# Performance work log

Measured on AMD Instinct MI355X. Metric: run time of the kernel, lower is better.

## Reference

```python
import jax, jax.numpy as jnp
import numpy as np

B, C, W, H = 4, 512, 64, 64
CK = C // 8  # channels // k


def setup_inputs() -> dict:
    key = jax.random.key(0)
    ks = jax.random.split(key, 10)
    s = 0.02
    return {
        "x": jax.random.normal(ks[0], (B, C, W, H), jnp.float32),
        "wf": jax.random.normal(ks[1], (CK, C), jnp.float32) * s,
        "bf": jax.random.normal(ks[2], (CK,), jnp.float32) * s,
        "wg": jax.random.normal(ks[3], (CK, C), jnp.float32) * s,
        "bg": jax.random.normal(ks[4], (CK,), jnp.float32) * s,
        "wh": jax.random.normal(ks[5], (CK, C), jnp.float32) * s,
        "bh": jax.random.normal(ks[6], (CK,), jnp.float32) * s,
        "wv": jax.random.normal(ks[7], (C, CK), jnp.float32) * s,
        "bv": jax.random.normal(ks[8], (C,), jnp.float32) * s,
        "gamma": jax.random.normal(ks[9], (1,), jnp.float32) * 0.1,
    }


def reference(x, wf, bf, wg, bg, wh, bh, wv, bv, gamma):
    b, c, w, h = x.shape
    n = w * h  # location_num
    xf = x.reshape(b, c, n)  # (B, C, N)
    # conv1x1 projections == per-location matmuls
    f = jnp.einsum('oc,bcn->bon', wf, xf) + bf[None, :, None]  # (B, CK, N)
    g = jnp.einsum('oc,bcn->bon', wg, xf) + bg[None, :, None]
    hh = jnp.einsum('oc,bcn->bon', wh, xf) + bh[None, :, None]
    # beta[b, i, j] = sum_c f[b,c,i] * g[b,c,j]; softmax over dim=1 (i axis)
    beta = jax.nn.softmax(jnp.einsum('bcn,bcm->bnm', f, g), axis=1)  # (B, N, N)
    h2 = jnp.einsum('bcn,bnm->bcm', hh, beta)  # (B, CK, N)
    o = jnp.einsum('oc,bcn->bon', wv, h2) + bv[None, :, None]  # (B, C, N)
    y = gamma[0] * o + xf
    return y.reshape(b, c, w, h)
```

## Files before the change

### kernel.cpp

```cpp
#include <hip/hip_runtime.h>
#include <stdint.h>

#define B_ 4
#define C_ 512
#define N_ 4096
#define D_ 64
#define LOG2E 1.4426950408889634f

typedef __attribute__((ext_vector_type(8))) short short8;
typedef __attribute__((ext_vector_type(4))) float f32x4;
typedef __attribute__((ext_vector_type(16))) float f32x16;
typedef unsigned short ushort_t;

static __device__ __forceinline__ ushort_t f2bf(float f) {
    union { float f; uint32_t u; } v; v.f = f;
    uint32_t u = v.u;
    uint32_t r = u + 0x7FFFu + ((u >> 16) & 1u);
    return (ushort_t)(r >> 16);
}
static __device__ __forceinline__ float bf2f(uint32_t u) {
    union { uint32_t u; float f; } v; v.u = u << 16;
    return v.f;
}
static __device__ __forceinline__ uint32_t cvtpk_bf16(float lo, float hi) {
    uint32_t r;
    asm("v_cvt_pk_bf16_f32 %0, %1, %2" : "=v"(r) : "v"(lo), "v"(hi));
    return r;
}
static __device__ __forceinline__ void gl16(const ushort_t* g, ushort_t* l) {
    __builtin_amdgcn_global_load_lds(
        (const __attribute__((address_space(1))) void*)g,
        (__attribute__((address_space(3))) void*)l, 16, 0, 0);
}

__global__ __launch_bounds__(512) void proj_fgh(
    const float* __restrict__ x,
    const float* __restrict__ wf, const float* __restrict__ bf,
    const float* __restrict__ wg, const float* __restrict__ bg,
    const float* __restrict__ wh, const float* __restrict__ bh,
    ushort_t* __restrict__ Ftf, ushort_t* __restrict__ Gt,
    ushort_t* __restrict__ Vtf)
{
    const int b    = blockIdx.y;
    const int tile = blockIdx.x;
    const int n0   = tile * 64;
    const int tid  = threadIdx.x;
    const int wv   = tid >> 6;
    const int mw   = wv & 3;
    const int hi   = wv >> 2;
    const int lane = tid & 63;
    const int g    = lane >> 4;
    const int r    = lane & 15;

    __shared__ ushort_t As[64][40];
    __shared__ ushort_t Bs[192][40];

    f32x4 acc[6];
    #pragma unroll
    for (int t = 0; t < 6; ++t) acc[t] = (f32x4){0.f, 0.f, 0.f, 0.f};

    const int ka = tid >> 4;
    const int mb = (tid & 15) * 4;
    const int kb = (tid & 7) * 4;
    const int ow = tid >> 3;

    const float* xp  = x  + ((size_t)b * C_ + ka) * N_ + n0 + mb;
    const float* wp0 = wf + (size_t)ow * C_ + kb;
    const float* wp1 = wg + (size_t)ow * C_ + kb;
    const float* wp2 = wh + (size_t)ow * C_ + kb;

    float4 xa = *(const float4*)xp;
    float4 w0 = *(const float4*)wp0;
    float4 w1 = *(const float4*)wp1;
    float4 w2 = *(const float4*)wp2;

    for (int k0 = 0; k0 < C_; k0 += 32) {
        As[mb + 0][ka] = f2bf(xa.x);
        As[mb + 1][ka] = f2bf(xa.y);
        As[mb + 2][ka] = f2bf(xa.z);
        As[mb + 3][ka] = f2bf(xa.w);
        {
            uint2 p0, p1, p2;
            p0.x = cvtpk_bf16(w0.x, w0.y); p0.y = cvtpk_bf16(w0.z, w0.w);
            p1.x = cvtpk_bf16(w1.x, w1.y); p1.y = cvtpk_bf16(w1.z, w1.w);
            p2.x = cvtpk_bf16(w2.x, w2.y); p2.y = cvtpk_bf16(w2.z, w2.w);
            *(uint2*)&Bs[ow][kb]       = p0;
            *(uint2*)&Bs[64 + ow][kb]  = p1;
            *(uint2*)&Bs[128 + ow][kb] = p2;
        }
        if (k0 + 32 < C_) {
            xa = *(const float4*)(xp + (size_t)(k0 + 32) * N_);
            w0 = *(const float4*)(wp0 + k0 + 32);
            w1 = *(const float4*)(wp1 + k0 + 32);
            w2 = *(const float4*)(wp2 + k0 + 32);
        }
        __syncthreads();
        short8 a = *(const short8*)&As[16 * mw + r][8 * g];
        __builtin_amdgcn_s_setprio(1);
        #pragma unroll
        for (int tt = 0; tt < 6; ++tt) {
            const int T = hi * 6 + tt;
            short8 bbv = *(const short8*)&Bs[T * 16 + r][8 * g];
            acc[tt] = __builtin_amdgcn_mfma_f32_16x16x32_bf16(a, bbv, acc[tt], 0, 0, 0);
        }
        __builtin_amdgcn_s_setprio(0);
        __syncthreads();
    }

    #pragma unroll
    for (int u = 0; u < 2; ++u) {
        const int tt = hi ? u : (4 + u);
        const int og = hi ? (32 + u * 16 + r) : (u * 16 + r);
        const float bvv = bg[og];
        #pragma unroll
        for (int j = 0; j < 4; ++j) {
            const int loc = n0 + 16 * mw + 4 * g + j;
            Gt[((size_t)b * N_ + loc) * D_ + og] = f2bf(acc[tt][j] + bvv);
        }
    }

    ushort_t (*bb)[72] = (ushort_t(*)[72])Bs;

    if (hi == 0) {
        #pragma unroll
        for (int tt = 0; tt < 4; ++tt) {
            const int o = tt * 16 + r;
            const float bvv = bf[o];
            #pragma unroll
            for (int j = 0; j < 4; ++j)
                bb[16 * mw + 4 * g + j][o] = f2bf((acc[tt][j] + bvv) * LOG2E);
        }
    }
    __syncthreads();
    {
        const int f  = wv;
        const int cc = f >> 2, s = f & 3;
        short8 v = *(const short8*)&bb[32 * cc + (lane & 31)][16 * s + 8 * (lane >> 5)];
        *(short8*)&Ftf[(((size_t)b * 64 + tile) * 8 + f) * 512 + lane * 8] = v;
    }
    __syncthreads();

    if (hi == 1) {
        #pragma unroll
        for (int tt = 2; tt < 6; ++tt) {
            const int o = (tt - 2) * 16 + r;
            const float bvv = bh[o];
            #pragma unroll
            for (int j = 0; j < 4; ++j)
                bb[16 * mw + 4 * g + j][o] = f2bf(acc[tt][j] + bvv);
        }
    }
    __syncthreads();
    {
        const int f   = wv;
        const int cc  = f >> 2, sub = (f >> 1) & 1, dt = f & 1;
        const int h2l = lane >> 5;
        short8 v;
        #pragma unroll
        for (int e = 0; e < 8; ++e) {
            const int i = 32 * cc + 16 * sub + (e & 3) + 8 * (e >> 2) + 4 * h2l;
            v[e] = (short)bb[i][32 * dt + (lane & 31)];
        }
        *(short8*)&Vtf[(((size_t)b * 64 + tile) * 8 + f) * 512 + lane * 8] = v;
    }
}

__global__ __launch_bounds__(256, 4) void attn(
    const ushort_t* __restrict__ Ftf, const ushort_t* __restrict__ Gt,
    const ushort_t* __restrict__ Vtf, ushort_t* __restrict__ Ot,
    ushort_t* __restrict__ Op, float* __restrict__ ml, int ksplit)
{
    const int b    = blockIdx.z;
    const int part = blockIdx.y;
    const int tid  = threadIdx.x;
    const int wave = tid >> 6;
    const int lane = tid & 63;
    const int l31  = lane & 31;
    const int h2   = lane >> 5;
    const int j0   = blockIdx.x * 128 + wave * 32;
    const int NT   = (N_ / ksplit) / 64;
    const int kt0  = part * NT;

    __shared__ __align__(16) ushort_t Ks[2][4096];
    __shared__ __align__(16) ushort_t Vs[2][4096];

    const ushort_t* qrow = Gt + ((size_t)b * N_ + j0 + l31) * D_ + 8 * h2;
    const short8 qf0 = *(const short8*)(qrow);
    const short8 qf1 = *(const short8*)(qrow + 16);
    const short8 qf2 = *(const short8*)(qrow + 32);
    const short8 qf3 = *(const short8*)(qrow + 48);

    const ushort_t* Kt = Ftf + ((size_t)b * 64 + kt0) * 4096;
    const ushort_t* Vt = Vtf + ((size_t)b * 64 + kt0) * 4096;

    f32x16 oA, oB;
    #pragma unroll
    for (int q = 0; q < 16; ++q) { oA[q] = 0.f; oB[q] = 0.f; }
    float l_run = 0.f;

    gl16(Kt + tid * 8,         &Ks[0][tid * 8]);
    gl16(Kt + (tid + 256) * 8, &Ks[0][(tid + 256) * 8]);
    gl16(Vt + tid * 8,         &Vs[0][tid * 8]);
    gl16(Vt + (tid + 256) * 8, &Vs[0][(tid + 256) * 8]);

    int buf = 0;
    for (int t = 0; t < NT; ++t) {
        __syncthreads();
        if (t + 1 < NT) {
            const ushort_t* kg = Kt + (size_t)(t + 1) * 4096;
            const ushort_t* vg = Vt + (size_t)(t + 1) * 4096;
            const int nb = buf ^ 1;
            gl16(kg + tid * 8,         &Ks[nb][tid * 8]);
            gl16(kg + (tid + 256) * 8, &Ks[nb][(tid + 256) * 8]);
            gl16(vg + tid * 8,         &Vs[nb][tid * 8]);
            gl16(vg + (tid + 256) * 8, &Vs[nb][(tid + 256) * 8]);
        }
        #pragma unroll
        for (int cc = 0; cc < 2; ++cc) {
            const ushort_t* kb0 = &Ks[buf][cc * 2048];
            f32x16 sx;
            #pragma unroll
            for (int q = 0; q < 16; ++q) sx[q] = 0.f;
            __builtin_amdgcn_s_setprio(1);
            {
                const short8 k0 = *(const short8*)(kb0 + 0 * 512 + lane * 8);
                sx = __builtin_amdgcn_mfma_f32_32x32x16_bf16(k0, qf0, sx, 0, 0, 0);
                const short8 k1 = *(const short8*)(kb0 + 1 * 512 + lane * 8);
                sx = __builtin_amdgcn_mfma_f32_32x32x16_bf16(k1, qf1, sx, 0, 0, 0);
                const short8 k2 = *(const short8*)(kb0 + 2 * 512 + lane * 8);
                sx = __builtin_amdgcn_mfma_f32_32x32x16_bf16(k2, qf2, sx, 0, 0, 0);
                const short8 k3 = *(const short8*)(kb0 + 3 * 512 + lane * 8);
                sx = __builtin_amdgcn_mfma_f32_32x32x16_bf16(k3, qf3, sx, 0, 0, 0);
            }
            __builtin_amdgcn_s_setprio(0);

            uint32_t pw[8];
            float cs = 0.f;
            #pragma unroll
            for (int q = 0; q < 8; ++q) {
                const float pa = __builtin_amdgcn_exp2f(sx[2 * q]);
                const float pb = __builtin_amdgcn_exp2f(sx[2 * q + 1]);
                cs += pa + pb;
                pw[q] = cvtpk_bf16(pa, pb);
            }
            l_run += cs;

            union { uint32_t w[4]; short8 v; } p0u, p1u;
            p0u.w[0] = pw[0]; p0u.w[1] = pw[1]; p0u.w[2] = pw[2]; p0u.w[3] = pw[3];
            p1u.w[0] = pw[4]; p1u.w[1] = pw[5]; p1u.w[2] = pw[6]; p1u.w[3] = pw[7];

            const ushort_t* vb0 = &Vs[buf][cc * 2048];
            __builtin_amdgcn_s_setprio(1);
            {
                const short8 v00 = *(const short8*)(vb0 + 0 * 512 + lane * 8);
                oA = __builtin_amdgcn_mfma_f32_32x32x16_bf16(v00, p0u.v, oA, 0, 0, 0);
                const short8 v01 = *(const short8*)(vb0 + 1 * 512 + lane * 8);
                oB = __builtin_amdgcn_mfma_f32_32x32x16_bf16(v01, p0u.v, oB, 0, 0, 0);
                const short8 v10 = *(const short8*)(vb0 + 2 * 512 + lane * 8);
                oA = __builtin_amdgcn_mfma_f32_32x32x16_bf16(v10, p1u.v, oA, 0, 0, 0);
                const short8 v11 = *(const short8*)(vb0 + 3 * 512 + lane * 8);
                oB = __builtin_amdgcn_mfma_f32_32x32x16_bf16(v11, p1u.v, oB, 0, 0, 0);
            }
            __builtin_amdgcn_s_setprio(0);
        }
        buf ^= 1;
    }

    const float lt = l_run + __shfl_xor(l_run, 32);

    if (ksplit == 1) {
        const float inv = 1.0f / lt;
        ushort_t* orow = Ot + ((size_t)b * N_ + j0 + l31) * D_;
        #pragma unroll
        for (int q = 0; q < 4; ++q) {
            const int d0 = 8 * q + 4 * h2;
            uint2 ua, ub;
            ua.x = cvtpk_bf16(oA[4 * q] * inv,     oA[4 * q + 1] * inv);
            ua.y = cvtpk_bf16(oA[4 * q + 2] * inv, oA[4 * q + 3] * inv);
            *(uint2*)&orow[d0] = ua;
            ub.x = cvtpk_bf16(oB[4 * q] * inv,     oB[4 * q + 1] * inv);
            ub.y = cvtpk_bf16(oB[4 * q + 2] * inv, oB[4 * q + 3] * inv);
            *(uint2*)&orow[32 + d0] = ub;
        }
    } else {
        ushort_t* orow = Op + (((size_t)b * ksplit + part) * N_ + j0 + l31) * D_;
        #pragma unroll
        for (int q = 0; q < 4; ++q) {
            const int d0 = 8 * q + 4 * h2;
            uint2 ua, ub;
            ua.x = cvtpk_bf16(oA[4 * q],     oA[4 * q + 1]);
            ua.y = cvtpk_bf16(oA[4 * q + 2], oA[4 * q + 3]);
            *(uint2*)&orow[d0] = ua;
            ub.x = cvtpk_bf16(oB[4 * q],     oB[4 * q + 1]);
            ub.y = cvtpk_bf16(oB[4 * q + 2], oB[4 * q + 3]);
            *(uint2*)&orow[32 + d0] = ub;
        }
        if (h2 == 0)
            ml[((size_t)b * ksplit + part) * N_ + j0 + l31] = lt;
    }
}

__global__ __launch_bounds__(256) void reduce_attn(
    const ushort_t* __restrict__ Op, const float* __restrict__ ml,
    ushort_t* __restrict__ Ot, int ksplit)
{
    const int tid = blockIdx.x * 256 + threadIdx.x;
    const int d4 = (tid & 15) * 4;
    const int j  = (tid >> 4) & (N_ - 1);
    const int b  = tid >> 16;

    float L = 0.f, v0 = 0.f, v1 = 0.f, v2 = 0.f, v3 = 0.f;
    for (int p = 0; p < ksplit; ++p) {
        const size_t base = ((size_t)b * ksplit + p) * N_ + j;
        L += ml[base];
        uint2 u = *(const uint2*)&Op[base * D_ + d4];
        v0 += bf2f(u.x & 0xffffu);
        v1 += bf2f(u.x >> 16);
        v2 += bf2f(u.y & 0xffffu);
        v3 += bf2f(u.y >> 16);
    }
    const float inv = 1.0f / L;
    uint2 o;
    o.x = cvtpk_bf16(v0 * inv, v1 * inv);
    o.y = cvtpk_bf16(v2 * inv, v3 * inv);
    *(uint2*)&Ot[((size_t)b * N_ + j) * D_ + d4] = o;
}

__global__ __launch_bounds__(256) void outproj(
    const ushort_t* __restrict__ Ot, const float* __restrict__ wv,
    const float* __restrict__ bv, const float* __restrict__ gamma,
    const float* __restrict__ x, float* __restrict__ y)
{
    const int b    = blockIdx.z;
    const int wave = threadIdx.x >> 6;
    const int lane = threadIdx.x & 63;
    const int g    = lane >> 4;
    const int r    = lane & 15;
    const int co0  = blockIdx.y * 64 + wave * 16;
    const int n0   = blockIdx.x * 64;

    const float* wrow = wv + (size_t)(co0 + r) * D_ + 8 * g;
    short8 a0, a1;
    #pragma unroll
    for (int j = 0; j < 8; ++j) {
        a0[j] = (short)f2bf(wrow[j]);
        a1[j] = (short)f2bf(wrow[32 + j]);
    }

    f32x4 acc[4];
    #pragma unroll
    for (int t = 0; t < 4; ++t) acc[t] = (f32x4){0.f, 0.f, 0.f, 0.f};

    #pragma unroll
    for (int t = 0; t < 4; ++t) {
        const ushort_t* op = Ot + ((size_t)b * N_ + n0 + 16 * t + r) * D_ + 8 * g;
        short8 b0 = *(const short8*)op;
        short8 b1 = *(const short8*)(op + 32);
        acc[t] = __builtin_amdgcn_mfma_f32_16x16x32_bf16(a0, b0, acc[t], 0, 0, 0);
        acc[t] = __builtin_amdgcn_mfma_f32_16x16x32_bf16(a1, b1, acc[t], 0, 0, 0);
    }

    const float gm = *gamma;
    #pragma unroll
    for (int t = 0; t < 4; ++t) {
        #pragma unroll
        for (int j = 0; j < 4; ++j) {
            const int co = co0 + 4 * g + j;
            const int n  = n0 + 16 * t + r;
            const size_t idx = ((size_t)b * C_ + co) * N_ + n;
            y[idx] = gm * (acc[t][j] + bv[co]) + x[idx];
        }
    }
}

extern "C" void kernel_launch(void* const* d_in, const int* in_sizes, int n_in,
                              void* d_out, int out_size, void* d_ws, size_t ws_size,
                              hipStream_t stream) {
    const float* x     = (const float*)d_in[0];
    const float* wf    = (const float*)d_in[1];
    const float* bf    = (const float*)d_in[2];
    const float* wg    = (const float*)d_in[3];
    const float* bg    = (const float*)d_in[4];
    const float* wh    = (const float*)d_in[5];
    const float* bh    = (const float*)d_in[6];
    const float* wv    = (const float*)d_in[7];
    const float* bv    = (const float*)d_in[8];
    const float* gamma = (const float*)d_in[9];
    float* y = (float*)d_out;

    const size_t plane = (size_t)B_ * N_ * D_;
    ushort_t* Ftf = (ushort_t*)d_ws;
    ushort_t* Gt  = Ftf + plane;
    ushort_t* Vtf = Gt + plane;
    ushort_t* Ot  = Vtf + plane;
    ushort_t* Op  = Ot + plane;

    int KS = 8;
    while (KS > 1) {
        const size_t need = 4 * plane * 2 + (size_t)KS * plane * 2
                          + (size_t)B_ * KS * N_ * sizeof(float);
        if (need <= ws_size) break;
        KS >>= 1;
    }
    float* ml = (float*)(Op + (size_t)KS * plane);

    proj_fgh<<<dim3(N_ / 64, B_), 512, 0, stream>>>(
        x, wf, bf, wg, bg, wh, bh, Ftf, Gt, Vtf);
    attn<<<dim3(N_ / 128, KS, B_), 256, 0, stream>>>(
        Ftf, Gt, Vtf, Ot, Op, ml, KS);
    if (KS > 1)
        reduce_attn<<<(B_ * N_ * 16) / 256, 256, 0, stream>>>(Op, ml, Ot, KS);
    outproj<<<dim3(N_ / 64, C_ / 64, B_), 256, 0, stream>>>(Ot, wv, bv, gamma, x, y);
}
```

Baseline: 65.47 us.

## Process two query tiles per wave in attention to reuse K/V LDS loads

Each wave now handles 64 query columns (two 32-wide tiles) instead of 32, so every K and V fragment read from shared memory feeds two MFMAs. The block covers 256 queries and the grid halves, cutting LDS and global K/V traffic per unit of work. Register pressure roughly doubles for accumulators, so launch bounds drop occupancy to 2 blocks per SIMD-group, and fewer blocks may underfill the GPU. The split-K reduce kernel is also widened to 8 bf16 elements per thread with 128-bit loads.

```diff
diff --git a/kernel.cpp b/kernel.cpp
--- a/kernel.cpp
+++ b/kernel.cpp
@@ -165,7 +165,7 @@
     }
 }
 
-__global__ __launch_bounds__(256, 4) void attn(
+__global__ __launch_bounds__(256, 2) void attn(
     const ushort_t* __restrict__ Ftf, const ushort_t* __restrict__ Gt,
     const ushort_t* __restrict__ Vtf, ushort_t* __restrict__ Ot,
     ushort_t* __restrict__ Op, float* __restrict__ ml, int ksplit)
@@ -177,26 +177,31 @@
     const int lane = tid & 63;
     const int l31  = lane & 31;
     const int h2   = lane >> 5;
-    const int j0   = blockIdx.x * 128 + wave * 32;
+    const int j0   = blockIdx.x * 256 + wave * 64;
     const int NT   = (N_ / ksplit) / 64;
     const int kt0  = part * NT;
 
     __shared__ __align__(16) ushort_t Ks[2][4096];
     __shared__ __align__(16) ushort_t Vs[2][4096];
 
-    const ushort_t* qrow = Gt + ((size_t)b * N_ + j0 + l31) * D_ + 8 * h2;
-    const short8 qf0 = *(const short8*)(qrow);
-    const short8 qf1 = *(const short8*)(qrow + 16);
-    const short8 qf2 = *(const short8*)(qrow + 32);
-    const short8 qf3 = *(const short8*)(qrow + 48);
+    const ushort_t* qrowA = Gt + ((size_t)b * N_ + j0 + l31) * D_ + 8 * h2;
+    const ushort_t* qrowB = qrowA + (size_t)32 * D_;
+    const short8 qA0 = *(const short8*)(qrowA);
+    const short8 qA1 = *(const short8*)(qrowA + 16);
+    const short8 qA2 = *(const short8*)(qrowA + 32);
+    const short8 qA3 = *(const short8*)(qrowA + 48);
+    const short8 qB0 = *(const short8*)(qrowB);
+    const short8 qB1 = *(const short8*)(qrowB + 16);
+    const short8 qB2 = *(const short8*)(qrowB + 32);
+    const short8 qB3 = *(const short8*)(qrowB + 48);
 
     const ushort_t* Kt = Ftf + ((size_t)b * 64 + kt0) * 4096;
     const ushort_t* Vt = Vtf + ((size_t)b * 64 + kt0) * 4096;
 
-    f32x16 oA, oB;
-    #pragma unroll
-    for (int q = 0; q < 16; ++q) { oA[q] = 0.f; oB[q] = 0.f; }
-    float l_run = 0.f;
+    f32x16 oAA, oBA, oAB, oBB;
+    #pragma unroll
+    for (int q = 0; q < 16; ++q) { oAA[q] = 0.f; oBA[q] = 0.f; oAB[q] = 0.f; oBB[q] = 0.f; }
+    float lA = 0.f, lB = 0.f;
 
     gl16(Kt + tid * 8,         &Ks[0][tid * 8]);
     gl16(Kt + (tid + 256) * 8, &Ks[0][(tid + 256) * 8]);
@@ -218,85 +223,119 @@
         #pragma unroll
         for (int cc = 0; cc < 2; ++cc) {
             const ushort_t* kb0 = &Ks[buf][cc * 2048];
-            f32x16 sx;
+            f32x16 sxA, sxB;
             #pragma unroll
-            for (int q = 0; q < 16; ++q) sx[q] = 0.f;
+            for (int q = 0; q < 16; ++q) { sxA[q] = 0.f; sxB[q] = 0.f; }
             __builtin_amdgcn_s_setprio(1);
             {
                 const short8 k0 = *(const short8*)(kb0 + 0 * 512 + lane * 8);
-                sx = __builtin_amdgcn_mfma_f32_32x32x16_bf16(k0, qf0, sx, 0, 0, 0);
+                sxA = __builtin_amdgcn_mfma_f32_32x32x16_bf16(k0, qA0, sxA, 0, 0, 0);
+                sxB = __builtin_amdgcn_mfma_f32_32x32x16_bf16(k0, qB0, sxB, 0, 0, 0);
                 const short8 k1 = *(const short8*)(kb0 + 1 * 512 + lane * 8);
-                sx = __builtin_amdgcn_mfma_f32_32x32x16_bf16(k1, qf1, sx, 0, 0, 0);
+                sxA = __builtin_amdgcn_mfma_f32_32x32x16_bf16(k1, qA1, sxA, 0, 0, 0);
+                sxB = __builtin_amdgcn_mfma_f32_32x32x16_bf16(k1, qB1, sxB, 0, 0, 0);
                 const short8 k2 = *(const short8*)(kb0 + 2 * 512 + lane * 8);
-                sx = __builtin_amdgcn_mfma_f32_32x32x16_bf16(k2, qf2, sx, 0, 0, 0);
+                sxA = __builtin_amdgcn_mfma_f32_32x32x16_bf16(k2, qA2, sxA, 0, 0, 0);
+                sxB = __builtin_amdgcn_mfma_f32_32x32x16_bf16(k2, qB2, sxB, 0, 0, 0);
                 const short8 k3 = *(const short8*)(kb0 + 3 * 512 + lane * 8);
-                sx = __builtin_amdgcn_mfma_f32_32x32x16_bf16(k3, qf3, sx, 0, 0, 0);
+                sxA = __builtin_amdgcn_mfma_f32_32x32x16_bf16(k3, qA3, sxA, 0, 0, 0);
+                sxB = __builtin_amdgcn_mfma_f32_32x32x16_bf16(k3, qB3, sxB, 0, 0, 0);
             }
             __builtin_amdgcn_s_setprio(0);
 
-            uint32_t pw[8];
-            float cs = 0.f;
+            uint32_t pwA[8], pwB[8];
+            float cA0 = 0.f, cA1 = 0.f, cB0 = 0.f, cB1 = 0.f;
             #pragma unroll
             for (int q = 0; q < 8; ++q) {
-                const float pa = __builtin_amdgcn_exp2f(sx[2 * q]);
-                const float pb = __builtin_amdgcn_exp2f(sx[2 * q + 1]);
-                cs += pa + pb;
-                pw[q] = cvtpk_bf16(pa, pb);
+                const float a0 = __builtin_amdgcn_exp2f(sxA[2 * q]);
+                const float a1 = __builtin_amdgcn_exp2f(sxA[2 * q + 1]);
+                cA0 += a0; cA1 += a1;
+                pwA[q] = cvtpk_bf16(a0, a1);
+                const float b0 = __builtin_amdgcn_exp2f(sxB[2 * q]);
+                const float b1 = __builtin_amdgcn_exp2f(sxB[2 * q + 1]);
+                cB0 += b0; cB1 += b1;
+                pwB[q] = cvtpk_bf16(b0, b1);
             }
-            l_run += cs;
-
-            union { uint32_t w[4]; short8 v; } p0u, p1u;
-            p0u.w[0] = pw[0]; p0u.w[1] = pw[1]; p0u.w[2] = pw[2]; p0u.w[3] = pw[3];
-            p1u.w[0] = pw[4]; p1u.w[1] = pw[5]; p1u.w[2] = pw[6]; p1u.w[3] = pw[7];
+            lA += cA0 + cA1;
+            lB += cB0 + cB1;
+
+            union { uint32_t w[4]; short8 v; } pA0u, pA1u, pB0u, pB1u;
+            pA0u.w[0] = pwA[0]; pA0u.w[1] = pwA[1]; pA0u.w[2] = pwA[2]; pA0u.w[3] = pwA[3];
+            pA1u.w[0] = pwA[4]; pA1u.w[1] = pwA[5]; pA1u.w[2] = pwA[6]; pA1u.w[3] = pwA[7];
+            pB0u.w[0] = pwB[0]; pB0u.w[1] = pwB[1]; pB0u.w[2] = pwB[2]; pB0u.w[3] = pwB[3];
+            pB1u.w[0] = pwB[4]; pB1u.w[1] = pwB[5]; pB1u.w[2] = pwB[6]; pB1u.w[3] = pwB[7];
 
             const ushort_t* vb0 = &Vs[buf][cc * 2048];
             __builtin_amdgcn_s_setprio(1);
             {
                 const short8 v00 = *(const short8*)(vb0 + 0 * 512 + lane * 8);
-                oA = __builtin_amdgcn_mfma_f32_32x32x16_bf16(v00, p0u.v, oA, 0, 0, 0);
+                oAA = __builtin_amdgcn_mfma_f32_32x32x16_bf16(v00, pA0u.v, oAA, 0, 0, 0);
+                oAB = __builtin_amdgcn_mfma_f32_32x32x16_bf16(v00, pB0u.v, oAB, 0, 0, 0);
                 const short8 v01 = *(const short8*)(vb0 + 1 * 512 + lane * 8);
-                oB = __builtin_amdgcn_mfma_f32_32x32x16_bf16(v01, p0u.v, oB, 0, 0, 0);
+                oBA = __builtin_amdgcn_mfma_f32_32x32x16_bf16(v01, pA0u.v, oBA, 0, 0, 0);
+                oBB = __builtin_amdgcn_mfma_f32_32x32x16_bf16(v01, pB0u.v, oBB, 0, 0, 0);
                 const short8 v10 = *(const short8*)(vb0 + 2 * 512 + lane * 8);
-                oA = __builtin_amdgcn_mfma_f32_32x32x16_bf16(v10, p1u.v, oA, 0, 0, 0);
+                oAA = __builtin_amdgcn_mfma_f32_32x32x16_bf16(v10, pA1u.v, oAA, 0, 0, 0);
+                oAB = __builtin_amdgcn_mfma_f32_32x32x16_bf16(v10, pB1u.v, oAB, 0, 0, 0);
                 const short8 v11 = *(const short8*)(vb0 + 3 * 512 + lane * 8);
-                oB = __builtin_amdgcn_mfma_f32_32x32x16_bf16(v11, p1u.v, oB, 0, 0, 0);
+                oBA = __builtin_amdgcn_mfma_f32_32x32x16_bf16(v11, pA1u.v, oBA, 0, 0, 0);
+                oBB = __builtin_amdgcn_mfma_f32_32x32x16_bf16(v11, pB1u.v, oBB, 0, 0, 0);
             }
             __builtin_amdgcn_s_setprio(0);
         }
         buf ^= 1;
     }
 
-    const float lt = l_run + __shfl_xor(l_run, 32);
+    const float ltA = lA + __shfl_xor(lA, 32);
+    const float ltB = lB + __shfl_xor(lB, 32);
 
     if (ksplit == 1) {
-        const float inv = 1.0f / lt;
-        ushort_t* orow = Ot + ((size_t)b * N_ + j0 + l31) * D_;
+        const float invA = 1.0f / ltA;
+        const float invB = 1.0f / ltB;
+        ushort_t* orowA = Ot + ((size_t)b * N_ + j0 + l31) * D_;
+        ushort_t* orowB = orowA + (size_t)32 * D_;
         #pragma unroll
         for (int q = 0; q < 4; ++q) {
             const int d0 = 8 * q + 4 * h2;
-            uint2 ua, ub;
-            ua.x = cvtpk_bf16(oA[4 * q] * inv,     oA[4 * q + 1] * inv);
-            ua.y = cvtpk_bf16(oA[4 * q + 2] * inv, oA[4 * q + 3] * inv);
-            *(uint2*)&orow[d0] = ua;
-            ub.x = cvtpk_bf16(oB[4 * q] * inv,     oB[4 * q + 1] * inv);
-            ub.y = cvtpk_bf16(oB[4 * q + 2] * inv, oB[4 * q + 3] * inv);
-            *(uint2*)&orow[32 + d0] = ub;
+            uint2 u;
+            u.x = cvtpk_bf16(oAA[4 * q] * invA,     oAA[4 * q + 1] * invA);
+            u.y = cvtpk_bf16(oAA[4 * q + 2] * invA, oAA[4 * q + 3] * invA);
+            *(uint2*)&orowA[d0] = u;
+            u.x = cvtpk_bf16(oBA[4 * q] * invA,     oBA[4 * q + 1] * invA);
+            u.y = cvtpk_bf16(oBA[4 * q + 2] * invA, oBA[4 * q + 3] * invA);
+            *(uint2*)&orowA[32 + d0] = u;
+            u.x = cvtpk_bf16(oAB[4 * q] * invB,     oAB[4 * q + 1] * invB);
+            u.y = cvtpk_bf16(oAB[4 * q + 2] * invB, oAB[4 * q + 3] * invB);
+            *(uint2*)&orowB[d0] = u;
+            u.x = cvtpk_bf16(oBB[4 * q] * invB,     oBB[4 * q + 1] * invB);
+            u.y = cvtpk_bf16(oBB[4 * q + 2] * invB, oBB[4 * q + 3] * invB);
+            *(uint2*)&orowB[32 + d0] = u;
         }
     } else {
-        ushort_t* orow = Op + (((size_t)b * ksplit + part) * N_ + j0 + l31) * D_;
+        ushort_t* orowA = Op + (((size_t)b * ksplit + part) * N_ + j0 + l31) * D_;
+        ushort_t* orowB = orowA + (size_t)32 * D_;
         #pragma unroll
         for (int q = 0; q < 4; ++q) {
             const int d0 = 8 * q + 4 * h2;
-            uint2 ua, ub;
-            ua.x = cvtpk_bf16(oA[4 * q],     oA[4 * q + 1]);
-            ua.y = cvtpk_bf16(oA[4 * q + 2], oA[4 * q + 3]);
-            *(uint2*)&orow[d0] = ua;
-            ub.x = cvtpk_bf16(oB[4 * q],     oB[4 * q + 1]);
-            ub.y = cvtpk_bf16(oB[4 * q + 2], oB[4 * q + 3]);
-            *(uint2*)&orow[32 + d0] = ub;
-        }
-        if (h2 == 0)
-            ml[((size_t)b * ksplit + part) * N_ + j0 + l31] = lt;
+            uint2 u;
+            u.x = cvtpk_bf16(oAA[4 * q],     oAA[4 * q + 1]);
+            u.y = cvtpk_bf16(oAA[4 * q + 2], oAA[4 * q + 3]);
+            *(uint2*)&orowA[d0] = u;
+            u.x = cvtpk_bf16(oBA[4 * q],     oBA[4 * q + 1]);
+            u.y = cvtpk_bf16(oBA[4 * q + 2], oBA[4 * q + 3]);
+            *(uint2*)&orowA[32 + d0] = u;
+            u.x = cvtpk_bf16(oAB[4 * q],     oAB[4 * q + 1]);
+            u.y = cvtpk_bf16(oAB[4 * q + 2], oAB[4 * q + 3]);
+            *(uint2*)&orowB[d0] = u;
+            u.x = cvtpk_bf16(oBB[4 * q],     oBB[4 * q + 1]);
+            u.y = cvtpk_bf16(oBB[4 * q + 2], oBB[4 * q + 3]);
+            *(uint2*)&orowB[32 + d0] = u;
+        }
+        if (h2 == 0) {
+            const size_t mbase = ((size_t)b * ksplit + part) * N_;
+            ml[mbase + j0 + l31]      = ltA;
+            ml[mbase + j0 + 32 + l31] = ltB;
+        }
     }
 }
 
@@ -305,25 +344,28 @@
     ushort_t* __restrict__ Ot, int ksplit)
 {
     const int tid = blockIdx.x * 256 + threadIdx.x;
-    const int d4 = (tid & 15) * 4;
-    const int j  = (tid >> 4) & (N_ - 1);
-    const int b  = tid >> 16;
-
-    float L = 0.f, v0 = 0.f, v1 = 0.f, v2 = 0.f, v3 = 0.f;
+    const int d8 = (tid & 7) * 8;
+    const int j  = (tid >> 3) & (N_ - 1);
+    const int b  = tid >> 15;
+
+    float L = 0.f;
+    float v[8] = {0.f, 0.f, 0.f, 0.f, 0.f, 0.f, 0.f, 0.f};
     for (int p = 0; p < ksplit; ++p) {
         const size_t base = ((size_t)b * ksplit + p) * N_ + j;
         L += ml[base];
-        uint2 u = *(const uint2*)&Op[base * D_ + d4];
-        v0 += bf2f(u.x & 0xffffu);
-        v1 += bf2f(u.x >> 16);
-        v2 += bf2f(u.y & 0xffffu);
-        v3 += bf2f(u.y >> 16);
+        uint4 u = *(const uint4*)&Op[base * D_ + d8];
+        v[0] += bf2f(u.x & 0xffffu); v[1] += bf2f(u.x >> 16);
+        v[2] += bf2f(u.y & 0xffffu); v[3] += bf2f(u.y >> 16);
+        v[4] += bf2f(u.z & 0xffffu); v[5] += bf2f(u.z >> 16);
+        v[6] += bf2f(u.w & 0xffffu); v[7] += bf2f(u.w >> 16);
     }
     const float inv = 1.0f / L;
-    uint2 o;
-    o.x = cvtpk_bf16(v0 * inv, v1 * inv);
-    o.y = cvtpk_bf16(v2 * inv, v3 * inv);
-    *(uint2*)&Ot[((size_t)b * N_ + j) * D_ + d4] = o;
+    uint4 o;
+    o.x = cvtpk_bf16(v[0] * inv, v[1] * inv);
+    o.y = cvtpk_bf16(v[2] * inv, v[3] * inv);
+    o.z = cvtpk_bf16(v[4] * inv, v[5] * inv);
+    o.w = cvtpk_bf16(v[6] * inv, v[7] * inv);
+    *(uint4*)&Ot[((size_t)b * N_ + j) * D_ + d8] = o;
 }
 
 __global__ __launch_bounds__(256) void outproj(
@@ -406,9 +448,9 @@
 
     proj_fgh<<<dim3(N_ / 64, B_), 512, 0, stream>>>(
         x, wf, bf, wg, bg, wh, bh, Ftf, Gt, Vtf);
-    attn<<<dim3(N_ / 128, KS, B_), 256, 0, stream>>>(
+    attn<<<dim3(N_ / 256, KS, B_), 256, 0, stream>>>(
         Ftf, Gt, Vtf, Ot, Op, ml, KS);
     if (KS > 1)
-        reduce_attn<<<(B_ * N_ * 16) / 256, 256, 0, stream>>>(Op, ml, Ot, KS);
+        reduce_attn<<<(B_ * N_ * 8) / 256, 256, 0, stream>>>(Op, ml, Ot, KS);
     outproj<<<dim3(N_ / 64, C_ / 64, B_), 256, 0, stream>>>(Ot, wv, bv, gamma, x, y);
 }
```

Result: slower. 66.78 us (+2.0%).

## Load K/V fragments directly from global memory instead of LDS staging

Applied to the files above, without the earlier changes.

The attention kernel drops the double-buffered LDS staging of K/V tiles (global_load_lds plus __syncthreads) and has each wave read its MFMA fragments straight from global memory in 32-key chunks, prefetching the next K fragment into registers. This removes block-wide barriers and LDS traffic, but every wave now re-reads the same K/V data through the cache hierarchy. Occupancy hint lowered from 4 to 3 blocks to allow more registers. The split-K reduction kernel is also widened to 16-byte loads and stores with half as many threads.

```diff
diff --git a/kernel.cpp b/kernel.cpp
--- a/kernel.cpp
+++ b/kernel.cpp
@@ -26,11 +26,6 @@
     uint32_t r;
     asm("v_cvt_pk_bf16_f32 %0, %1, %2" : "=v"(r) : "v"(lo), "v"(hi));
     return r;
-}
-static __device__ __forceinline__ void gl16(const ushort_t* g, ushort_t* l) {
-    __builtin_amdgcn_global_load_lds(
-        (const __attribute__((address_space(1))) void*)g,
-        (__attribute__((address_space(3))) void*)l, 16, 0, 0);
 }
 
 __global__ __launch_bounds__(512) void proj_fgh(
@@ -165,7 +160,7 @@
     }
 }
 
-__global__ __launch_bounds__(256, 4) void attn(
+__global__ __launch_bounds__(256, 3) void attn(
     const ushort_t* __restrict__ Ftf, const ushort_t* __restrict__ Gt,
     const ushort_t* __restrict__ Vtf, ushort_t* __restrict__ Ot,
     ushort_t* __restrict__ Op, float* __restrict__ ml, int ksplit)
@@ -178,11 +173,8 @@
     const int l31  = lane & 31;
     const int h2   = lane >> 5;
     const int j0   = blockIdx.x * 128 + wave * 32;
-    const int NT   = (N_ / ksplit) / 64;
-    const int kt0  = part * NT;
-
-    __shared__ __align__(16) ushort_t Ks[2][4096];
-    __shared__ __align__(16) ushort_t Vs[2][4096];
+    const int NC   = (N_ / ksplit) / 32;
+    const int c0   = part * NC;
 
     const ushort_t* qrow = Gt + ((size_t)b * N_ + j0 + l31) * D_ + 8 * h2;
     const short8 qf0 = *(const short8*)(qrow);
@@ -190,80 +182,65 @@
     const short8 qf2 = *(const short8*)(qrow + 32);
     const short8 qf3 = *(const short8*)(qrow + 48);
 
-    const ushort_t* Kt = Ftf + ((size_t)b * 64 + kt0) * 4096;
-    const ushort_t* Vt = Vtf + ((size_t)b * 64 + kt0) * 4096;
+    const ushort_t* Kc = Ftf + (size_t)b * (N_ * D_) + (size_t)c0 * 2048 + lane * 8;
+    const ushort_t* Vc = Vtf + (size_t)b * (N_ * D_) + (size_t)c0 * 2048 + lane * 8;
 
     f32x16 oA, oB;
     #pragma unroll
     for (int q = 0; q < 16; ++q) { oA[q] = 0.f; oB[q] = 0.f; }
     float l_run = 0.f;
 
-    gl16(Kt + tid * 8,         &Ks[0][tid * 8]);
-    gl16(Kt + (tid + 256) * 8, &Ks[0][(tid + 256) * 8]);
-    gl16(Vt + tid * 8,         &Vs[0][tid * 8]);
-    gl16(Vt + (tid + 256) * 8, &Vs[0][(tid + 256) * 8]);
-
-    int buf = 0;
-    for (int t = 0; t < NT; ++t) {
-        __syncthreads();
-        if (t + 1 < NT) {
-            const ushort_t* kg = Kt + (size_t)(t + 1) * 4096;
-            const ushort_t* vg = Vt + (size_t)(t + 1) * 4096;
-            const int nb = buf ^ 1;
-            gl16(kg + tid * 8,         &Ks[nb][tid * 8]);
-            gl16(kg + (tid + 256) * 8, &Ks[nb][(tid + 256) * 8]);
-            gl16(vg + tid * 8,         &Vs[nb][tid * 8]);
-            gl16(vg + (tid + 256) * 8, &Vs[nb][(tid + 256) * 8]);
-        }
-        #pragma unroll
-        for (int cc = 0; cc < 2; ++cc) {
-            const ushort_t* kb0 = &Ks[buf][cc * 2048];
-            f32x16 sx;
-            #pragma unroll
-            for (int q = 0; q < 16; ++q) sx[q] = 0.f;
-            __builtin_amdgcn_s_setprio(1);
-            {
-                const short8 k0 = *(const short8*)(kb0 + 0 * 512 + lane * 8);
-                sx = __builtin_amdgcn_mfma_f32_32x32x16_bf16(k0, qf0, sx, 0, 0, 0);
-                const short8 k1 = *(const short8*)(kb0 + 1 * 512 + lane * 8);
-                sx = __builtin_amdgcn_mfma_f32_32x32x16_bf16(k1, qf1, sx, 0, 0, 0);
-                const short8 k2 = *(const short8*)(kb0 + 2 * 512 + lane * 8);
-                sx = __builtin_amdgcn_mfma_f32_32x32x16_bf16(k2, qf2, sx, 0, 0, 0);
-                const short8 k3 = *(const short8*)(kb0 + 3 * 512 + lane * 8);
-                sx = __builtin_amdgcn_mfma_f32_32x32x16_bf16(k3, qf3, sx, 0, 0, 0);
-            }
-            __builtin_amdgcn_s_setprio(0);
-
-            uint32_t pw[8];
-            float cs = 0.f;
-            #pragma unroll
-            for (int q = 0; q < 8; ++q) {
-                const float pa = __builtin_amdgcn_exp2f(sx[2 * q]);
-                const float pb = __builtin_amdgcn_exp2f(sx[2 * q + 1]);
-                cs += pa + pb;
-                pw[q] = cvtpk_bf16(pa, pb);
-            }
-            l_run += cs;
-
-            union { uint32_t w[4]; short8 v; } p0u, p1u;
-            p0u.w[0] = pw[0]; p0u.w[1] = pw[1]; p0u.w[2] = pw[2]; p0u.w[3] = pw[3];
-            p1u.w[0] = pw[4]; p1u.w[1] = pw[5]; p1u.w[2] = pw[6]; p1u.w[3] = pw[7];
-
-            const ushort_t* vb0 = &Vs[buf][cc * 2048];
-            __builtin_amdgcn_s_setprio(1);
-            {
-                const short8 v00 = *(const short8*)(vb0 + 0 * 512 + lane * 8);
-                oA = __builtin_amdgcn_mfma_f32_32x32x16_bf16(v00, p0u.v, oA, 0, 0, 0);
-                const short8 v01 = *(const short8*)(vb0 + 1 * 512 + lane * 8);
-                oB = __builtin_amdgcn_mfma_f32_32x32x16_bf16(v01, p0u.v, oB, 0, 0, 0);
-                const short8 v10 = *(const short8*)(vb0 + 2 * 512 + lane * 8);
-                oA = __builtin_amdgcn_mfma_f32_32x32x16_bf16(v10, p1u.v, oA, 0, 0, 0);
-                const short8 v11 = *(const short8*)(vb0 + 3 * 512 + lane * 8);
-                oB = __builtin_amdgcn_mfma_f32_32x32x16_bf16(v11, p1u.v, oB, 0, 0, 0);
-            }
-            __builtin_amdgcn_s_setprio(0);
-        }
-        buf ^= 1;
+    short8 k0 = *(const short8*)(Kc);
+    short8 k1 = *(const short8*)(Kc + 512);
+    short8 k2 = *(const short8*)(Kc + 1024);
+    short8 k3 = *(const short8*)(Kc + 1536);
+
+    for (int c = 0; c < NC; ++c) {
+        const ushort_t* vp = Vc + (size_t)c * 2048;
+        const short8 v00 = *(const short8*)(vp);
+        const short8 v01 = *(const short8*)(vp + 512);
+        const short8 v10 = *(const short8*)(vp + 1024);
+        const short8 v11 = *(const short8*)(vp + 1536);
+
+        f32x16 sx;
+        #pragma unroll
+        for (int q = 0; q < 16; ++q) sx[q] = 0.f;
+        __builtin_amdgcn_s_setprio(1);
+        sx = __builtin_amdgcn_mfma_f32_32x32x16_bf16(k0, qf0, sx, 0, 0, 0);
+        sx = __builtin_amdgcn_mfma_f32_32x32x16_bf16(k1, qf1, sx, 0, 0, 0);
+        sx = __builtin_amdgcn_mfma_f32_32x32x16_bf16(k2, qf2, sx, 0, 0, 0);
+        sx = __builtin_amdgcn_mfma_f32_32x32x16_bf16(k3, qf3, sx, 0, 0, 0);
+        __builtin_amdgcn_s_setprio(0);
+
+        if (c + 1 < NC) {
+            const ushort_t* kp = Kc + (size_t)(c + 1) * 2048;
+            k0 = *(const short8*)(kp);
+            k1 = *(const short8*)(kp + 512);
+            k2 = *(const short8*)(kp + 1024);
+            k3 = *(const short8*)(kp + 1536);
+        }
+
+        uint32_t pw[8];
+        float cs = 0.f;
+        #pragma unroll
+        for (int q = 0; q < 8; ++q) {
+            const float pa = __builtin_amdgcn_exp2f(sx[2 * q]);
+            const float pb = __builtin_amdgcn_exp2f(sx[2 * q + 1]);
+            cs += pa + pb;
+            pw[q] = cvtpk_bf16(pa, pb);
+        }
+        l_run += cs;
+
+        union { uint32_t w[4]; short8 v; } p0u, p1u;
+        p0u.w[0] = pw[0]; p0u.w[1] = pw[1]; p0u.w[2] = pw[2]; p0u.w[3] = pw[3];
+        p1u.w[0] = pw[4]; p1u.w[1] = pw[5]; p1u.w[2] = pw[6]; p1u.w[3] = pw[7];
+
+        __builtin_amdgcn_s_setprio(1);
+        oA = __builtin_amdgcn_mfma_f32_32x32x16_bf16(v00, p0u.v, oA, 0, 0, 0);
+        oB = __builtin_amdgcn_mfma_f32_32x32x16_bf16(v01, p0u.v, oB, 0, 0, 0);
+        oA = __builtin_amdgcn_mfma_f32_32x32x16_bf16(v10, p1u.v, oA, 0, 0, 0);
+        oB = __builtin_amdgcn_mfma_f32_32x32x16_bf16(v11, p1u.v, oB, 0, 0, 0);
+        __builtin_amdgcn_s_setprio(0);
     }
 
     const float lt = l_run + __shfl_xor(l_run, 32);
@@ -305,25 +282,28 @@
     ushort_t* __restrict__ Ot, int ksplit)
 {
     const int tid = blockIdx.x * 256 + threadIdx.x;
-    const int d4 = (tid & 15) * 4;
-    const int j  = (tid >> 4) & (N_ - 1);
-    const int b  = tid >> 16;
-
-    float L = 0.f, v0 = 0.f, v1 = 0.f, v2 = 0.f, v3 = 0.f;
+    const int d8 = (tid & 7) * 8;
+    const int j  = (tid >> 3) & (N_ - 1);
+    const int b  = tid >> 15;
+
+    float L = 0.f;
+    float v[8] = {0.f, 0.f, 0.f, 0.f, 0.f, 0.f, 0.f, 0.f};
     for (int p = 0; p < ksplit; ++p) {
         const size_t base = ((size_t)b * ksplit + p) * N_ + j;
         L += ml[base];
-        uint2 u = *(const uint2*)&Op[base * D_ + d4];
-        v0 += bf2f(u.x & 0xffffu);
-        v1 += bf2f(u.x >> 16);
-        v2 += bf2f(u.y & 0xffffu);
-        v3 += bf2f(u.y >> 16);
+        uint4 u = *(const uint4*)&Op[base * D_ + d8];
+        v[0] += bf2f(u.x & 0xffffu); v[1] += bf2f(u.x >> 16);
+        v[2] += bf2f(u.y & 0xffffu); v[3] += bf2f(u.y >> 16);
+        v[4] += bf2f(u.z & 0xffffu); v[5] += bf2f(u.z >> 16);
+        v[6] += bf2f(u.w & 0xffffu); v[7] += bf2f(u.w >> 16);
     }
     const float inv = 1.0f / L;
-    uint2 o;
-    o.x = cvtpk_bf16(v0 * inv, v1 * inv);
-    o.y = cvtpk_bf16(v2 * inv, v3 * inv);
-    *(uint2*)&Ot[((size_t)b * N_ + j) * D_ + d4] = o;
+    uint4 o;
+    o.x = cvtpk_bf16(v[0] * inv, v[1] * inv);
+    o.y = cvtpk_bf16(v[2] * inv, v[3] * inv);
+    o.z = cvtpk_bf16(v[4] * inv, v[5] * inv);
+    o.w = cvtpk_bf16(v[6] * inv, v[7] * inv);
+    *(uint4*)&Ot[((size_t)b * N_ + j) * D_ + d8] = o;
 }
 
 __global__ __launch_bounds__(256) void outproj(
@@ -409,6 +389,6 @@
     attn<<<dim3(N_ / 128, KS, B_), 256, 0, stream>>>(
         Ftf, Gt, Vtf, Ot, Op, ml, KS);
     if (KS > 1)
-        reduce_attn<<<(B_ * N_ * 16) / 256, 256, 0, stream>>>(Op, ml, Ot, KS);
+        reduce_attn<<<(B_ * N_ * 8) / 256, 256, 0, stream>>>(Op, ml, Ot, KS);
     outproj<<<dim3(N_ / 64, C_ / 64, B_), 256, 0, stream>>>(Ot, wv, bv, gamma, x, y);
 }
```

Measured after the change: 66.49 us. No clear change (+1.6%).

## Fuse split-K reduction into output projection kernel via shared-memory tile

Applied to the files above, without the earlier changes.

Merges reduce_attn and outproj into one kernel. Each 512-thread block first reduces the split-K partial outputs for 64 locations into an LDS tile, then all 8 waves run the output projection over all 512 channels from that tile. This removes one launch and the global round-trip of the normalized attention output, and loads each Op row once per block instead of once per channel block. In exchange the grid shrinks to 256 blocks, and each wave holds more accumulators, which raises register pressure.

```diff
diff --git a/kernel.cpp b/kernel.cpp
--- a/kernel.cpp
+++ b/kernel.cpp
@@ -167,14 +167,14 @@
 
 __global__ __launch_bounds__(256, 4) void attn(
     const ushort_t* __restrict__ Ftf, const ushort_t* __restrict__ Gt,
-    const ushort_t* __restrict__ Vtf, ushort_t* __restrict__ Ot,
+    const ushort_t* __restrict__ Vtf,
     ushort_t* __restrict__ Op, float* __restrict__ ml, int ksplit)
 {
     const int b    = blockIdx.z;
     const int part = blockIdx.y;
     const int tid  = threadIdx.x;
+    const int lane = tid & 63;
     const int wave = tid >> 6;
-    const int lane = tid & 63;
     const int l31  = lane & 31;
     const int h2   = lane >> 5;
     const int j0   = blockIdx.x * 128 + wave * 32;
@@ -268,107 +268,109 @@
 
     const float lt = l_run + __shfl_xor(l_run, 32);
 
-    if (ksplit == 1) {
-        const float inv = 1.0f / lt;
-        ushort_t* orow = Ot + ((size_t)b * N_ + j0 + l31) * D_;
-        #pragma unroll
-        for (int q = 0; q < 4; ++q) {
-            const int d0 = 8 * q + 4 * h2;
-            uint2 ua, ub;
-            ua.x = cvtpk_bf16(oA[4 * q] * inv,     oA[4 * q + 1] * inv);
-            ua.y = cvtpk_bf16(oA[4 * q + 2] * inv, oA[4 * q + 3] * inv);
-            *(uint2*)&orow[d0] = ua;
-            ub.x = cvtpk_bf16(oB[4 * q] * inv,     oB[4 * q + 1] * inv);
-            ub.y = cvtpk_bf16(oB[4 * q + 2] * inv, oB[4 * q + 3] * inv);
-            *(uint2*)&orow[32 + d0] = ub;
-        }
-    } else {
-        ushort_t* orow = Op + (((size_t)b * ksplit + part) * N_ + j0 + l31) * D_;
-        #pragma unroll
-        for (int q = 0; q < 4; ++q) {
-            const int d0 = 8 * q + 4 * h2;
-            uint2 ua, ub;
-            ua.x = cvtpk_bf16(oA[4 * q],     oA[4 * q + 1]);
-            ua.y = cvtpk_bf16(oA[4 * q + 2], oA[4 * q + 3]);
-            *(uint2*)&orow[d0] = ua;
-            ub.x = cvtpk_bf16(oB[4 * q],     oB[4 * q + 1]);
-            ub.y = cvtpk_bf16(oB[4 * q + 2], oB[4 * q + 3]);
-            *(uint2*)&orow[32 + d0] = ub;
-        }
-        if (h2 == 0)
-            ml[((size_t)b * ksplit + part) * N_ + j0 + l31] = lt;
-    }
-}
-
-__global__ __launch_bounds__(256) void reduce_attn(
+    ushort_t* orow = Op + (((size_t)b * ksplit + part) * N_ + j0 + l31) * D_;
+    #pragma unroll
+    for (int q = 0; q < 4; ++q) {
+        const int d0 = 8 * q + 4 * h2;
+        uint2 ua, ub;
+        ua.x = cvtpk_bf16(oA[4 * q],     oA[4 * q + 1]);
+        ua.y = cvtpk_bf16(oA[4 * q + 2], oA[4 * q + 3]);
+        *(uint2*)&orow[d0] = ua;
+        ub.x = cvtpk_bf16(oB[4 * q],     oB[4 * q + 1]);
+        ub.y = cvtpk_bf16(oB[4 * q + 2], oB[4 * q + 3]);
+        *(uint2*)&orow[32 + d0] = ub;
+    }
+    if (h2 == 0)
+        ml[((size_t)b * ksplit + part) * N_ + j0 + l31] = lt;
+}
+
+__global__ __launch_bounds__(512) void reduce_outproj(
     const ushort_t* __restrict__ Op, const float* __restrict__ ml,
-    ushort_t* __restrict__ Ot, int ksplit)
+    const float* __restrict__ wv, const float* __restrict__ bv,
+    const float* __restrict__ gamma, const float* __restrict__ x,
+    float* __restrict__ y, int ksplit)
 {
-    const int tid = blockIdx.x * 256 + threadIdx.x;
-    const int d4 = (tid & 15) * 4;
-    const int j  = (tid >> 4) & (N_ - 1);
-    const int b  = tid >> 16;
-
-    float L = 0.f, v0 = 0.f, v1 = 0.f, v2 = 0.f, v3 = 0.f;
-    for (int p = 0; p < ksplit; ++p) {
-        const size_t base = ((size_t)b * ksplit + p) * N_ + j;
-        L += ml[base];
-        uint2 u = *(const uint2*)&Op[base * D_ + d4];
-        v0 += bf2f(u.x & 0xffffu);
-        v1 += bf2f(u.x >> 16);
-        v2 += bf2f(u.y & 0xffffu);
-        v3 += bf2f(u.y >> 16);
-    }
-    const float inv = 1.0f / L;
-    uint2 o;
-    o.x = cvtpk_bf16(v0 * inv, v1 * inv);
-    o.y = cvtpk_bf16(v2 * inv, v3 * inv);
-    *(uint2*)&Ot[((size_t)b * N_ + j) * D_ + d4] = o;
-}
-
-__global__ __launch_bounds__(256) void outproj(
-    const ushort_t* __restrict__ Ot, const float* __restrict__ wv,
-    const float* __restrict__ bv, const float* __restrict__ gamma,
-    const float* __restrict__ x, float* __restrict__ y)
-{
-    const int b    = blockIdx.z;
-    const int wave = threadIdx.x >> 6;
-    const int lane = threadIdx.x & 63;
+    const int b    = blockIdx.y;
+    const int n0   = blockIdx.x * 64;
+    const int tid  = threadIdx.x;
+    const int wv8  = tid >> 6;
+    const int lane = tid & 63;
     const int g    = lane >> 4;
     const int r    = lane & 15;
-    const int co0  = blockIdx.y * 64 + wave * 16;
-    const int n0   = blockIdx.x * 64;
-
-    const float* wrow = wv + (size_t)(co0 + r) * D_ + 8 * g;
-    short8 a0, a1;
-    #pragma unroll
-    for (int j = 0; j < 8; ++j) {
-        a0[j] = (short)f2bf(wrow[j]);
-        a1[j] = (short)f2bf(wrow[32 + j]);
-    }
-
-    f32x4 acc[4];
-    #pragma unroll
-    for (int t = 0; t < 4; ++t) acc[t] = (f32x4){0.f, 0.f, 0.f, 0.f};
+
+    __shared__ ushort_t Os[64][72];
+
+    {
+        const int loc = tid >> 3;
+        const int k8  = (tid & 7) * 8;
+        float L = 0.f;
+        float v[8] = {0.f, 0.f, 0.f, 0.f, 0.f, 0.f, 0.f, 0.f};
+        for (int p = 0; p < ksplit; ++p) {
+            const size_t base = ((size_t)b * ksplit + p) * N_ + n0 + loc;
+            L += ml[base];
+            uint4 u = *(const uint4*)&Op[base * D_ + k8];
+            v[0] += bf2f(u.x & 0xffffu); v[1] += bf2f(u.x >> 16);
+            v[2] += bf2f(u.y & 0xffffu); v[3] += bf2f(u.y >> 16);
+            v[4] += bf2f(u.z & 0xffffu); v[5] += bf2f(u.z >> 16);
+            v[6] += bf2f(u.w & 0xffffu); v[7] += bf2f(u.w >> 16);
+        }
+        const float inv = 1.0f / L;
+        uint4 o;
+        o.x = cvtpk_bf16(v[0] * inv, v[1] * inv);
+        o.y = cvtpk_bf16(v[2] * inv, v[3] * inv);
+        o.z = cvtpk_bf16(v[4] * inv, v[5] * inv);
+        o.w = cvtpk_bf16(v[6] * inv, v[7] * inv);
+        *(uint4*)&Os[loc][k8] = o;
+    }
+    __syncthreads();
+
+    short8 a[4][2];
+    #pragma unroll
+    for (int cs = 0; cs < 4; ++cs) {
+        const float* wrow = wv + (size_t)(wv8 * 64 + cs * 16 + r) * D_ + 8 * g;
+        const float4 wa = *(const float4*)(wrow);
+        const float4 wb = *(const float4*)(wrow + 4);
+        const float4 wc = *(const float4*)(wrow + 32);
+        const float4 wd = *(const float4*)(wrow + 36);
+        uint32_t* a0 = (uint32_t*)&a[cs][0];
+        uint32_t* a1 = (uint32_t*)&a[cs][1];
+        a0[0] = cvtpk_bf16(wa.x, wa.y); a0[1] = cvtpk_bf16(wa.z, wa.w);
+        a0[2] = cvtpk_bf16(wb.x, wb.y); a0[3] = cvtpk_bf16(wb.z, wb.w);
+        a1[0] = cvtpk_bf16(wc.x, wc.y); a1[1] = cvtpk_bf16(wc.z, wc.w);
+        a1[2] = cvtpk_bf16(wd.x, wd.y); a1[3] = cvtpk_bf16(wd.z, wd.w);
+    }
+
+    f32x4 acc[4][4];
+    #pragma unroll
+    for (int cs = 0; cs < 4; ++cs)
+        #pragma unroll
+        for (int t = 0; t < 4; ++t) acc[cs][t] = (f32x4){0.f, 0.f, 0.f, 0.f};
 
     #pragma unroll
     for (int t = 0; t < 4; ++t) {
-        const ushort_t* op = Ot + ((size_t)b * N_ + n0 + 16 * t + r) * D_ + 8 * g;
-        short8 b0 = *(const short8*)op;
-        short8 b1 = *(const short8*)(op + 32);
-        acc[t] = __builtin_amdgcn_mfma_f32_16x16x32_bf16(a0, b0, acc[t], 0, 0, 0);
-        acc[t] = __builtin_amdgcn_mfma_f32_16x16x32_bf16(a1, b1, acc[t], 0, 0, 0);
+        const short8 b0 = *(const short8*)&Os[16 * t + r][8 * g];
+        const short8 b1 = *(const short8*)&Os[16 * t + r][32 + 8 * g];
+        __builtin_amdgcn_s_setprio(1);
+        #pragma unroll
+        for (int cs = 0; cs < 4; ++cs) {
+            acc[cs][t] = __builtin_amdgcn_mfma_f32_16x16x32_bf16(a[cs][0], b0, acc[cs][t], 0, 0, 0);
+            acc[cs][t] = __builtin_amdgcn_mfma_f32_16x16x32_bf16(a[cs][1], b1, acc[cs][t], 0, 0, 0);
+        }
+        __builtin_amdgcn_s_setprio(0);
     }
 
     const float gm = *gamma;
     #pragma unroll
-    for (int t = 0; t < 4; ++t) {
-        #pragma unroll
-        for (int j = 0; j < 4; ++j) {
-            const int co = co0 + 4 * g + j;
-            const int n  = n0 + 16 * t + r;
-            const size_t idx = ((size_t)b * C_ + co) * N_ + n;
-            y[idx] = gm * (acc[t][j] + bv[co]) + x[idx];
+    for (int cs = 0; cs < 4; ++cs) {
+        #pragma unroll
+        for (int t = 0; t < 4; ++t) {
+            #pragma unroll
+            for (int j = 0; j < 4; ++j) {
+                const int co = wv8 * 64 + cs * 16 + 4 * g + j;
+                const int n  = n0 + 16 * t + r;
+                const size_t idx = ((size_t)b * C_ + co) * N_ + n;
+                y[idx] = gm * (acc[cs][t][j] + bv[co]) + x[idx];
+            }
         }
     }
 }
@@ -392,12 +394,11 @@
     ushort_t* Ftf = (ushort_t*)d_ws;
     ushort_t* Gt  = Ftf + plane;
     ushort_t* Vtf = Gt + plane;
-    ushort_t* Ot  = Vtf + plane;
-    ushort_t* Op  = Ot + plane;
+    ushort_t* Op  = Vtf + plane;
 
     int KS = 8;
     while (KS > 1) {
-        const size_t need = 4 * plane * 2 + (size_t)KS * plane * 2
+        const size_t need = 3 * plane * 2 + (size_t)KS * plane * 2
                           + (size_t)B_ * KS * N_ * sizeof(float);
         if (need <= ws_size) break;
         KS >>= 1;
@@ -407,8 +408,7 @@
     proj_fgh<<<dim3(N_ / 64, B_), 512, 0, stream>>>(
         x, wf, bf, wg, bg, wh, bh, Ftf, Gt, Vtf);
     attn<<<dim3(N_ / 128, KS, B_), 256, 0, stream>>>(
-        Ftf, Gt, Vtf, Ot, Op, ml, KS);
-    if (KS > 1)
-        reduce_attn<<<(B_ * N_ * 16) / 256, 256, 0, stream>>>(Op, ml, Ot, KS);
-    outproj<<<dim3(N_ / 64, C_ / 64, B_), 256, 0, stream>>>(Ot, wv, bv, gamma, x, y);
-}
+        Ftf, Gt, Vtf, Op, ml, KS);
+    reduce_outproj<<<dim3(N_ / 64, B_), 512, 0, stream>>>(
+        Op, ml, wv, bv, gamma, x, y, KS);
+}
```

Result: faster. 60.11 us (-8.2%).
